# Kernel optimization log

Measured on AMD Instinct MI355X. Metric: run time of the kernel, lower is better.

The kernel has to match this reference:

```python
import jax, jax.numpy as jnp
import numpy as np

# Module hyperparameters (from __init__ defaults / init_kwargs)
A_PLUS = 0.005
A_MINUS = 0.00525
TAU_PLUS = 20.0
TAU_MINUS = 20.0
DT = 1.0

B, T, N_PRE, N_POST = 512, 100, 256, 256
SPIKE_RATE = 0.1


def setup_inputs() -> dict:
    key = jax.random.key(0)
    k1, k2, k3 = jax.random.split(key, 3)
    pre_spikes = (jax.random.uniform(k1, (B, T, N_PRE)) < SPIKE_RATE).astype(jnp.float32)
    post_spikes = (jax.random.uniform(k2, (B, T, N_POST)) < SPIKE_RATE).astype(jnp.float32)
    weights = jax.random.uniform(k3, (N_PRE, N_POST), dtype=jnp.float32)
    return {"pre_spikes": pre_spikes, "post_spikes": post_spikes, "weights": weights}


def _pre_trace(pre_tbn, decay):
    """trace[t] = sum_{tau=1..t} decay^tau * pre[t-tau]  (exact recurrence).

    pre_tbn: [T, B, N]. Returns [T, B, N] with trace[0] = 0.
    """
    def step(carry, x_t):
        # emit trace[t] = carry, then carry' = decay * (carry + pre[t])
        return decay * (carry + x_t), carry
    _, trace = jax.lax.scan(step, jnp.zeros_like(pre_tbn[0]), pre_tbn)
    return trace


def reference(pre_spikes, post_spikes, weights):
    """Classical STDP weight update.

    With T <= int(tau_plus*5) the original nested t/tau loops equal:
      dW[p,q] = (1/(B*T)) * sum_{t,b} (A+ * trace+[t,b,p] - A- * trace-[t,b,p]) * post[b,t,q]
    where trace+/- are exponential pre-synaptic eligibility traces.
    """
    batch, time_steps, _ = pre_spikes.shape
    pre_t = jnp.transpose(pre_spikes, (1, 0, 2))    # [T, B, n_pre]
    post_t = jnp.transpose(post_spikes, (1, 0, 2))  # [T, B, n_post]

    decay_plus = jnp.exp(jnp.float32(-DT / TAU_PLUS))
    decay_minus = jnp.exp(jnp.float32(-DT / TAU_MINUS))

    trace_plus = _pre_trace(pre_t, decay_plus)    # LTP: pre fires before post
    trace_minus = _pre_trace(pre_t, decay_minus)  # LTD: pre fires before post (depression of reversed pairing)

    eff = A_PLUS * trace_plus - A_MINUS * trace_minus  # [T, B, n_pre]
    weight_update = jnp.einsum('tbp,tbq->pq', eff, post_t) / (batch * time_steps)
    # original initializes update as zeros_like(weights); output shape matches weights
    return weight_update + jnp.zeros_like(weights)
```

## Files before the change

kernel.cpp:

```cpp
#include <hip/hip_runtime.h>
#include <stdint.h>

#define B_SZ   512
#define T_SZ   100
#define NPRE   256
#define NPOST  256
#define KTOT   (B_SZ * T_SZ)

typedef __bf16 bf16x8 __attribute__((ext_vector_type(8)));
typedef float  floatx4 __attribute__((ext_vector_type(4)));

__device__ __forceinline__ uint32_t bf16_rne(float v) {
    uint32_t bits = __float_as_uint(v);
    return (bits + 0x7FFFu + ((bits >> 16) & 1u)) >> 16;
}
__device__ __forceinline__ uint32_t pack_trunc2(float a, float b) {
    return (__float_as_uint(a) >> 16) | (__float_as_uint(b) & 0xFFFF0000u);
}

__global__ __launch_bounds__(512) void stdp_fused_gemm(
    const float* __restrict__ pre, const float* __restrict__ post,
    float* __restrict__ partial)
{
    __shared__ __align__(16) unsigned short A_lds[32][512];
    __shared__ __align__(16) unsigned short B_lds[64][512];

    const int bx = blockIdx.x;
    const int s  = bx & 127;
    const int pt = bx >> 7;
    const int tid = threadIdx.x;
    const int lane = tid & 63, wave = tid >> 6;
    const int wp = wave & 3, wq = wave >> 2;
    const int l15 = lane & 15, l4 = lane >> 4;

    const int p_loc = tid & 127, lbo = tid >> 7;
    uint32_t pk[50];
    {
        const int b = s * 4 + lbo;
        const float decay = 0.95122942450071400910f;
        const float* src = pre + (size_t)b * (T_SZ * NPRE) + pt * 128 + p_loc;
        float carry = 0.0f;
#pragma unroll
        for (int kc = 0; kc < 3; ++kc) {
            float x[32];
#pragma unroll
            for (int j = 0; j < 32; ++j)
                x[j] = src[(size_t)(kc * 32 + j) * NPRE];
#pragma unroll
            for (int j = 0; j < 16; ++j) {
                uint32_t lo = bf16_rne(carry);
                carry = decay * (carry + x[2 * j]);
                uint32_t hi = bf16_rne(carry);
                carry = decay * (carry + x[2 * j + 1]);
                pk[kc * 16 + j] = lo | (hi << 16);
            }
        }
        float x[4];
#pragma unroll
        for (int j = 0; j < 4; ++j)
            x[j] = src[(size_t)(96 + j) * NPRE];
#pragma unroll
        for (int j = 0; j < 2; ++j) {
            uint32_t lo = bf16_rne(carry);
            carry = decay * (carry + x[2 * j]);
            uint32_t hi = bf16_rne(carry);
            carry = decay * (carry + x[2 * j + 1]);
            pk[48 + j] = lo | (hi << 16);
        }
    }

    const int q = tid & 255, hh = tid >> 8;
    const int qg = q >> 4, q15 = q & 15;

    floatx4 acc[2][8] = {};

    for (int lb = 0; lb < 4; ++lb) {
        const int b = s * 4 + lb;

        if (lbo == lb) {
            const int pg = p_loc >> 4, lp = p_loc & 15;
#pragma unroll
            for (int kc = 0; kc < 3; ++kc)
#pragma unroll
                for (int l4w = 0; l4w < 4; ++l4w)
                    *(uint4*)&A_lds[kc * 8 + pg][(l4w * 16 + lp) * 8] =
                        make_uint4(pk[kc * 16 + l4w * 4], pk[kc * 16 + l4w * 4 + 1],
                                   pk[kc * 16 + l4w * 4 + 2], pk[kc * 16 + l4w * 4 + 3]);
            *(uint4*)&A_lds[24 + pg][lp * 8] = make_uint4(pk[48], pk[49], 0u, 0u);
#pragma unroll
            for (int l4w = 1; l4w < 4; ++l4w)
                *(uint4*)&A_lds[24 + pg][(l4w * 16 + lp) * 8] =
                    make_uint4(0u, 0u, 0u, 0u);
        }

        const float* pb = post + (size_t)b * (T_SZ * NPOST) + q;
        if (hh == 0) {
#pragma unroll
            for (int half = 0; half < 2; ++half) {
                float x[32];
#pragma unroll
                for (int j = 0; j < 32; ++j)
                    x[j] = pb[(size_t)(half * 32 + j) * NPOST];
#pragma unroll
                for (int o = 0; o < 4; ++o) {
                    int oct = half * 4 + o;
                    uint4 v = make_uint4(pack_trunc2(x[o * 8 + 0], x[o * 8 + 1]),
                                         pack_trunc2(x[o * 8 + 2], x[o * 8 + 3]),
                                         pack_trunc2(x[o * 8 + 4], x[o * 8 + 5]),
                                         pack_trunc2(x[o * 8 + 6], x[o * 8 + 7]));
                    *(uint4*)&B_lds[(oct >> 2) * 16 + qg][(((oct & 3) * 16 + q15)) * 8] = v;
                }
            }
        } else {
            float x[32];
#pragma unroll
            for (int j = 0; j < 32; ++j)
                x[j] = pb[(size_t)(64 + j) * NPOST];
            float y[4];
#pragma unroll
            for (int j = 0; j < 4; ++j)
                y[j] = pb[(size_t)(96 + j) * NPOST];
#pragma unroll
            for (int o = 0; o < 4; ++o) {
                int oct = 8 + o;
                uint4 v = make_uint4(pack_trunc2(x[o * 8 + 0], x[o * 8 + 1]),
                                     pack_trunc2(x[o * 8 + 2], x[o * 8 + 3]),
                                     pack_trunc2(x[o * 8 + 4], x[o * 8 + 5]),
                                     pack_trunc2(x[o * 8 + 6], x[o * 8 + 7]));
                *(uint4*)&B_lds[(oct >> 2) * 16 + qg][(((oct & 3) * 16 + q15)) * 8] = v;
            }
            *(uint4*)&B_lds[3 * 16 + qg][(q15) * 8] =
                make_uint4(pack_trunc2(y[0], y[1]), pack_trunc2(y[2], y[3]), 0u, 0u);
#pragma unroll
            for (int o = 13; o < 16; ++o)
                *(uint4*)&B_lds[3 * 16 + qg][(((o & 3) * 16 + q15)) * 8] =
                    make_uint4(0u, 0u, 0u, 0u);
        }
        __syncthreads();

#pragma unroll
        for (int kc = 0; kc < 4; ++kc) {
            bf16x8 a[2], bb[8];
#pragma unroll
            for (int f = 0; f < 2; ++f)
                a[f] = *(const bf16x8*)&A_lds[kc * 8 + wp * 2 + f][lane * 8];
#pragma unroll
            for (int g = 0; g < 8; ++g)
                bb[g] = *(const bf16x8*)&B_lds[kc * 16 + wq * 8 + g][lane * 8];
#pragma unroll
            for (int f = 0; f < 2; ++f)
#pragma unroll
                for (int g = 0; g < 8; ++g)
                    acc[f][g] = __builtin_amdgcn_mfma_f32_16x16x32_bf16(
                        a[f], bb[g], acc[f][g], 0, 0, 0);
        }
        __syncthreads();
    }

    float* pout = partial + (size_t)bx * (128 * 256);
#pragma unroll
    for (int f = 0; f < 2; ++f) {
        int r0 = wp * 32 + f * 16 + l4 * 4;
#pragma unroll
        for (int g = 0; g < 8; ++g) {
            int c = wq * 128 + g * 16 + l15;
#pragma unroll
            for (int v = 0; v < 4; ++v)
                pout[(size_t)(r0 + v) * 256 + c] = acc[f][g][v];
        }
    }
}

__global__ __launch_bounds__(256) void stdp_reduce1(
    const float* __restrict__ partial, float* __restrict__ tmp)
{
    const int t = blockIdx.x * 256 + threadIdx.x;
    const int g = t >> 16;
    const int e = t & 65535;
    const int pt = e >> 15;
    const float* src = partial + ((size_t)(pt * 128 + g * 16)) * 32768 + (e & 32767);
    float a4[4] = {};
#pragma unroll
    for (int i = 0; i < 4; ++i)
#pragma unroll
        for (int u = 0; u < 4; ++u)
            a4[u] += src[(size_t)(u * 4 + i) * 32768];
    tmp[t] = (a4[0] + a4[1]) + (a4[2] + a4[3]);
}

__global__ __launch_bounds__(256) void stdp_reduce2(
    const float* __restrict__ tmp, float* __restrict__ out)
{
    const int idx = blockIdx.x * 256 + threadIdx.x;
    float a[4];
#pragma unroll
    for (int u = 0; u < 4; ++u)
        a[u] = tmp[(size_t)(2 * u) * 65536 + idx] +
               tmp[(size_t)(2 * u + 1) * 65536 + idx];
    const float scale = (0.005f - 0.00525f) * (1.0f / (float)KTOT);
    out[idx] = ((a[0] + a[1]) + (a[2] + a[3])) * scale;
}

extern "C" void kernel_launch(void* const* d_in, const int* in_sizes, int n_in,
                              void* d_out, int out_size, void* d_ws, size_t ws_size,
                              hipStream_t stream)
{
    const float* pre  = (const float*)d_in[0];
    const float* post = (const float*)d_in[1];
    float* out = (float*)d_out;

    float* partial = (float*)d_ws;
    float* tmp     = (float*)((char*)d_ws + (size_t)33554432);

    stdp_fused_gemm<<<256, 512, 0, stream>>>(pre, post, partial);
    stdp_reduce1<<<2048, 256, 0, stream>>>(partial, tmp);
    stdp_reduce2<<<256, 256, 0, stream>>>(tmp, out);
}
```

Before: 144.6 us.

## Halve B LDS tile and split K loop into two phases for occupancy

The post-spike B tile in LDS is halved by loading and consuming time steps in two phases of 64 and 36 per batch, each followed by two MFMA k-chunks. A launch bound of 4 blocks per CU is added to push register use down. The goal is lower LDS and register footprint per block so more blocks fit per CU, and shorter register live ranges for the loaded post values. In exchange each batch iteration now needs two extra barriers, and the register cap may cause spills given the 50-entry packed trace array.

```diff
diff --git a/kernel.cpp b/kernel.cpp
--- a/kernel.cpp
+++ b/kernel.cpp
@@ -18,12 +18,12 @@
     return (__float_as_uint(a) >> 16) | (__float_as_uint(b) & 0xFFFF0000u);
 }
 
-__global__ __launch_bounds__(512) void stdp_fused_gemm(
+__global__ __launch_bounds__(512, 4) void stdp_fused_gemm(
     const float* __restrict__ pre, const float* __restrict__ post,
     float* __restrict__ partial)
 {
     __shared__ __align__(16) unsigned short A_lds[32][512];
-    __shared__ __align__(16) unsigned short B_lds[64][512];
+    __shared__ __align__(16) unsigned short B_lds[32][512];
 
     const int bx = blockIdx.x;
     const int s  = bx & 127;
@@ -76,6 +76,7 @@
 
     for (int lb = 0; lb < 4; ++lb) {
         const int b = s * 4 + lb;
+        const float* pb = post + (size_t)b * (T_SZ * NPOST) + q;
 
         if (lbo == lb) {
             const int pg = p_loc >> 4, lp = p_loc & 15;
@@ -92,58 +93,69 @@
                 *(uint4*)&A_lds[24 + pg][(l4w * 16 + lp) * 8] =
                     make_uint4(0u, 0u, 0u, 0u);
         }
-
-        const float* pb = post + (size_t)b * (T_SZ * NPOST) + q;
+        {
+            float x[32];
+#pragma unroll
+            for (int j = 0; j < 32; ++j)
+                x[j] = pb[(size_t)(hh * 32 + j) * NPOST];
+#pragma unroll
+            for (int o = 0; o < 4; ++o)
+                *(uint4*)&B_lds[hh * 16 + qg][(o * 16 + q15) * 8] =
+                    make_uint4(pack_trunc2(x[o * 8 + 0], x[o * 8 + 1]),
+                               pack_trunc2(x[o * 8 + 2], x[o * 8 + 3]),
+                               pack_trunc2(x[o * 8 + 4], x[o * 8 + 5]),
+                               pack_trunc2(x[o * 8 + 6], x[o * 8 + 7]));
+        }
+        __syncthreads();
+#pragma unroll
+        for (int kc = 0; kc < 2; ++kc) {
+            bf16x8 a[2], bb[8];
+#pragma unroll
+            for (int f = 0; f < 2; ++f)
+                a[f] = *(const bf16x8*)&A_lds[kc * 8 + wp * 2 + f][lane * 8];
+#pragma unroll
+            for (int g = 0; g < 8; ++g)
+                bb[g] = *(const bf16x8*)&B_lds[kc * 16 + wq * 8 + g][lane * 8];
+#pragma unroll
+            for (int f = 0; f < 2; ++f)
+#pragma unroll
+                for (int g = 0; g < 8; ++g)
+                    acc[f][g] = __builtin_amdgcn_mfma_f32_16x16x32_bf16(
+                        a[f], bb[g], acc[f][g], 0, 0, 0);
+        }
+        __syncthreads();
+
         if (hh == 0) {
-#pragma unroll
-            for (int half = 0; half < 2; ++half) {
-                float x[32];
-#pragma unroll
-                for (int j = 0; j < 32; ++j)
-                    x[j] = pb[(size_t)(half * 32 + j) * NPOST];
-#pragma unroll
-                for (int o = 0; o < 4; ++o) {
-                    int oct = half * 4 + o;
-                    uint4 v = make_uint4(pack_trunc2(x[o * 8 + 0], x[o * 8 + 1]),
-                                         pack_trunc2(x[o * 8 + 2], x[o * 8 + 3]),
-                                         pack_trunc2(x[o * 8 + 4], x[o * 8 + 5]),
-                                         pack_trunc2(x[o * 8 + 6], x[o * 8 + 7]));
-                    *(uint4*)&B_lds[(oct >> 2) * 16 + qg][(((oct & 3) * 16 + q15)) * 8] = v;
-                }
-            }
-        } else {
             float x[32];
 #pragma unroll
             for (int j = 0; j < 32; ++j)
                 x[j] = pb[(size_t)(64 + j) * NPOST];
+#pragma unroll
+            for (int o = 0; o < 4; ++o)
+                *(uint4*)&B_lds[qg][(o * 16 + q15) * 8] =
+                    make_uint4(pack_trunc2(x[o * 8 + 0], x[o * 8 + 1]),
+                               pack_trunc2(x[o * 8 + 2], x[o * 8 + 3]),
+                               pack_trunc2(x[o * 8 + 4], x[o * 8 + 5]),
+                               pack_trunc2(x[o * 8 + 6], x[o * 8 + 7]));
+        } else {
             float y[4];
 #pragma unroll
             for (int j = 0; j < 4; ++j)
                 y[j] = pb[(size_t)(96 + j) * NPOST];
-#pragma unroll
-            for (int o = 0; o < 4; ++o) {
-                int oct = 8 + o;
-                uint4 v = make_uint4(pack_trunc2(x[o * 8 + 0], x[o * 8 + 1]),
-                                     pack_trunc2(x[o * 8 + 2], x[o * 8 + 3]),
-                                     pack_trunc2(x[o * 8 + 4], x[o * 8 + 5]),
-                                     pack_trunc2(x[o * 8 + 6], x[o * 8 + 7]));
-                *(uint4*)&B_lds[(oct >> 2) * 16 + qg][(((oct & 3) * 16 + q15)) * 8] = v;
-            }
-            *(uint4*)&B_lds[3 * 16 + qg][(q15) * 8] =
+            *(uint4*)&B_lds[16 + qg][(q15) * 8] =
                 make_uint4(pack_trunc2(y[0], y[1]), pack_trunc2(y[2], y[3]), 0u, 0u);
 #pragma unroll
-            for (int o = 13; o < 16; ++o)
-                *(uint4*)&B_lds[3 * 16 + qg][(((o & 3) * 16 + q15)) * 8] =
+            for (int o = 1; o < 4; ++o)
+                *(uint4*)&B_lds[16 + qg][(o * 16 + q15) * 8] =
                     make_uint4(0u, 0u, 0u, 0u);
         }
         __syncthreads();
-
-#pragma unroll
-        for (int kc = 0; kc < 4; ++kc) {
+#pragma unroll
+        for (int kc = 0; kc < 2; ++kc) {
             bf16x8 a[2], bb[8];
 #pragma unroll
             for (int f = 0; f < 2; ++f)
-                a[f] = *(const bf16x8*)&A_lds[kc * 8 + wp * 2 + f][lane * 8];
+                a[f] = *(const bf16x8*)&A_lds[(kc + 2) * 8 + wp * 2 + f][lane * 8];
 #pragma unroll
             for (int g = 0; g < 8; ++g)
                 bb[g] = *(const bf16x8*)&B_lds[kc * 16 + wq * 8 + g][lane * 8];
```

Measured after the change: 177.8 us. 22.9% more time.

## Split GEMM into 128x128 output tiles with 256-thread blocks and 2-block occupancy

Applied to the files above, without the earlier changes.

The fused trace+GEMM kernel now uses 512 blocks of 256 threads. Each block computes a 128x128 output tile, with P and Q tiles indexed from the block id, instead of a 128x256 tile. LDS per block is halved and launch bounds request two blocks per CU. The goal is more parallelism and better latency hiding. The cost is that the pre-trace recurrence is recomputed for both Q tiles and threads do two rounds of trace work, with the reduce kernels remapped to the new partial layout.

```diff
diff --git a/kernel.cpp b/kernel.cpp
--- a/kernel.cpp
+++ b/kernel.cpp
@@ -18,155 +18,151 @@
     return (__float_as_uint(a) >> 16) | (__float_as_uint(b) & 0xFFFF0000u);
 }
 
-__global__ __launch_bounds__(512) void stdp_fused_gemm(
+__global__ __launch_bounds__(256, 2) void stdp_fused_gemm(
     const float* __restrict__ pre, const float* __restrict__ post,
     float* __restrict__ partial)
 {
     __shared__ __align__(16) unsigned short A_lds[32][512];
-    __shared__ __align__(16) unsigned short B_lds[64][512];
-
-    const int bx = blockIdx.x;
-    const int s  = bx & 127;
-    const int pt = bx >> 7;
-    const int tid = threadIdx.x;
+    __shared__ __align__(16) unsigned short B_lds[32][512];
+
+    const int bx   = blockIdx.x;
+    const int s    = bx & 127;
+    const int tile = bx >> 7;
+    const int pt   = tile & 1;
+    const int qt   = tile >> 1;
+    const int tid  = threadIdx.x;
     const int lane = tid & 63, wave = tid >> 6;
-    const int wp = wave & 3, wq = wave >> 2;
     const int l15 = lane & 15, l4 = lane >> 4;
 
-    const int p_loc = tid & 127, lbo = tid >> 7;
-    uint32_t pk[50];
-    {
-        const int b = s * 4 + lbo;
-        const float decay = 0.95122942450071400910f;
-        const float* src = pre + (size_t)b * (T_SZ * NPRE) + pt * 128 + p_loc;
-        float carry = 0.0f;
-#pragma unroll
-        for (int kc = 0; kc < 3; ++kc) {
-            float x[32];
-#pragma unroll
-            for (int j = 0; j < 32; ++j)
-                x[j] = src[(size_t)(kc * 32 + j) * NPRE];
-#pragma unroll
-            for (int j = 0; j < 16; ++j) {
+    const int half  = tid >> 7;
+    const int p_loc = tid & 127;
+    const int qloc  = tid & 127;
+    const int qg = qloc >> 4, q15 = qloc & 15;
+
+    const float decay = 0.95122942450071400910f;
+
+    floatx4 acc[2][8] = {};
+
+    for (int r = 0; r < 2; ++r) {
+        uint32_t pk[50];
+        {
+            const int b = s * 4 + 2 * r + half;
+            const float* src = pre + (size_t)b * (T_SZ * NPRE) + pt * 128 + p_loc;
+            float carry = 0.0f;
+#pragma unroll
+            for (int kc = 0; kc < 3; ++kc) {
+                float x[32];
+#pragma unroll
+                for (int j = 0; j < 32; ++j)
+                    x[j] = src[(size_t)(kc * 32 + j) * NPRE];
+#pragma unroll
+                for (int j = 0; j < 16; ++j) {
+                    uint32_t lo = bf16_rne(carry);
+                    carry = decay * (carry + x[2 * j]);
+                    uint32_t hi = bf16_rne(carry);
+                    carry = decay * (carry + x[2 * j + 1]);
+                    pk[kc * 16 + j] = lo | (hi << 16);
+                }
+            }
+            float x[4];
+#pragma unroll
+            for (int j = 0; j < 4; ++j)
+                x[j] = src[(size_t)(96 + j) * NPRE];
+#pragma unroll
+            for (int j = 0; j < 2; ++j) {
                 uint32_t lo = bf16_rne(carry);
                 carry = decay * (carry + x[2 * j]);
                 uint32_t hi = bf16_rne(carry);
                 carry = decay * (carry + x[2 * j + 1]);
-                pk[kc * 16 + j] = lo | (hi << 16);
+                pk[48 + j] = lo | (hi << 16);
             }
         }
-        float x[4];
-#pragma unroll
-        for (int j = 0; j < 4; ++j)
-            x[j] = src[(size_t)(96 + j) * NPRE];
-#pragma unroll
-        for (int j = 0; j < 2; ++j) {
-            uint32_t lo = bf16_rne(carry);
-            carry = decay * (carry + x[2 * j]);
-            uint32_t hi = bf16_rne(carry);
-            carry = decay * (carry + x[2 * j + 1]);
-            pk[48 + j] = lo | (hi << 16);
+
+        for (int lh = 0; lh < 2; ++lh) {
+            const int b = s * 4 + 2 * r + lh;
+
+            if (half == lh) {
+                const int pg = p_loc >> 4, lp = p_loc & 15;
+#pragma unroll
+                for (int kc = 0; kc < 3; ++kc)
+#pragma unroll
+                    for (int w = 0; w < 4; ++w)
+                        *(uint4*)&A_lds[kc * 8 + pg][(w * 16 + lp) * 8] =
+                            make_uint4(pk[kc * 16 + w * 4],     pk[kc * 16 + w * 4 + 1],
+                                       pk[kc * 16 + w * 4 + 2], pk[kc * 16 + w * 4 + 3]);
+                *(uint4*)&A_lds[24 + pg][lp * 8] = make_uint4(pk[48], pk[49], 0u, 0u);
+#pragma unroll
+                for (int w = 1; w < 4; ++w)
+                    *(uint4*)&A_lds[24 + pg][(w * 16 + lp) * 8] =
+                        make_uint4(0u, 0u, 0u, 0u);
+            }
+
+            const float* pb = post + (size_t)b * (T_SZ * NPOST) + qt * 128 + qloc;
+            if (half == 0) {
+                float x[48];
+#pragma unroll
+                for (int j = 0; j < 48; ++j)
+                    x[j] = pb[(size_t)j * NPOST];
+#pragma unroll
+                for (int o = 0; o < 6; ++o)
+                    *(uint4*)&B_lds[(o >> 2) * 8 + qg][((o & 3) * 16 + q15) * 8] =
+                        make_uint4(pack_trunc2(x[o * 8 + 0], x[o * 8 + 1]),
+                                   pack_trunc2(x[o * 8 + 2], x[o * 8 + 3]),
+                                   pack_trunc2(x[o * 8 + 4], x[o * 8 + 5]),
+                                   pack_trunc2(x[o * 8 + 6], x[o * 8 + 7]));
+            } else {
+                float x[52];
+#pragma unroll
+                for (int j = 0; j < 52; ++j)
+                    x[j] = pb[(size_t)(48 + j) * NPOST];
+#pragma unroll
+                for (int o = 6; o < 12; ++o) {
+                    int u = o * 8 - 48;
+                    *(uint4*)&B_lds[(o >> 2) * 8 + qg][((o & 3) * 16 + q15) * 8] =
+                        make_uint4(pack_trunc2(x[u + 0], x[u + 1]),
+                                   pack_trunc2(x[u + 2], x[u + 3]),
+                                   pack_trunc2(x[u + 4], x[u + 5]),
+                                   pack_trunc2(x[u + 6], x[u + 7]));
+                }
+                *(uint4*)&B_lds[24 + qg][q15 * 8] =
+                    make_uint4(pack_trunc2(x[48], x[49]), pack_trunc2(x[50], x[51]), 0u, 0u);
+#pragma unroll
+                for (int o = 13; o < 16; ++o)
+                    *(uint4*)&B_lds[24 + qg][((o & 3) * 16 + q15) * 8] =
+                        make_uint4(0u, 0u, 0u, 0u);
+            }
+            __syncthreads();
+
+#pragma unroll
+            for (int kc = 0; kc < 4; ++kc) {
+                bf16x8 a[2], bb[8];
+#pragma unroll
+                for (int f = 0; f < 2; ++f)
+                    a[f] = *(const bf16x8*)&A_lds[kc * 8 + wave * 2 + f][lane * 8];
+#pragma unroll
+                for (int g = 0; g < 8; ++g)
+                    bb[g] = *(const bf16x8*)&B_lds[kc * 8 + g][lane * 8];
+#pragma unroll
+                for (int f = 0; f < 2; ++f)
+#pragma unroll
+                    for (int g = 0; g < 8; ++g)
+                        acc[f][g] = __builtin_amdgcn_mfma_f32_16x16x32_bf16(
+                            a[f], bb[g], acc[f][g], 0, 0, 0);
+            }
+            __syncthreads();
         }
     }
 
-    const int q = tid & 255, hh = tid >> 8;
-    const int qg = q >> 4, q15 = q & 15;
-
-    floatx4 acc[2][8] = {};
-
-    for (int lb = 0; lb < 4; ++lb) {
-        const int b = s * 4 + lb;
-
-        if (lbo == lb) {
-            const int pg = p_loc >> 4, lp = p_loc & 15;
-#pragma unroll
-            for (int kc = 0; kc < 3; ++kc)
-#pragma unroll
-                for (int l4w = 0; l4w < 4; ++l4w)
-                    *(uint4*)&A_lds[kc * 8 + pg][(l4w * 16 + lp) * 8] =
-                        make_uint4(pk[kc * 16 + l4w * 4], pk[kc * 16 + l4w * 4 + 1],
-                                   pk[kc * 16 + l4w * 4 + 2], pk[kc * 16 + l4w * 4 + 3]);
-            *(uint4*)&A_lds[24 + pg][lp * 8] = make_uint4(pk[48], pk[49], 0u, 0u);
-#pragma unroll
-            for (int l4w = 1; l4w < 4; ++l4w)
-                *(uint4*)&A_lds[24 + pg][(l4w * 16 + lp) * 8] =
-                    make_uint4(0u, 0u, 0u, 0u);
-        }
-
-        const float* pb = post + (size_t)b * (T_SZ * NPOST) + q;
-        if (hh == 0) {
-#pragma unroll
-            for (int half = 0; half < 2; ++half) {
-                float x[32];
-#pragma unroll
-                for (int j = 0; j < 32; ++j)
-                    x[j] = pb[(size_t)(half * 32 + j) * NPOST];
-#pragma unroll
-                for (int o = 0; o < 4; ++o) {
-                    int oct = half * 4 + o;
-                    uint4 v = make_uint4(pack_trunc2(x[o * 8 + 0], x[o * 8 + 1]),
-                                         pack_trunc2(x[o * 8 + 2], x[o * 8 + 3]),
-                                         pack_trunc2(x[o * 8 + 4], x[o * 8 + 5]),
-                                         pack_trunc2(x[o * 8 + 6], x[o * 8 + 7]));
-                    *(uint4*)&B_lds[(oct >> 2) * 16 + qg][(((oct & 3) * 16 + q15)) * 8] = v;
-                }
-            }
-        } else {
-            float x[32];
-#pragma unroll
-            for (int j = 0; j < 32; ++j)
-                x[j] = pb[(size_t)(64 + j) * NPOST];
-            float y[4];
-#pragma unroll
-            for (int j = 0; j < 4; ++j)
-                y[j] = pb[(size_t)(96 + j) * NPOST];
-#pragma unroll
-            for (int o = 0; o < 4; ++o) {
-                int oct = 8 + o;
-                uint4 v = make_uint4(pack_trunc2(x[o * 8 + 0], x[o * 8 + 1]),
-                                     pack_trunc2(x[o * 8 + 2], x[o * 8 + 3]),
-                                     pack_trunc2(x[o * 8 + 4], x[o * 8 + 5]),
-                                     pack_trunc2(x[o * 8 + 6], x[o * 8 + 7]));
-                *(uint4*)&B_lds[(oct >> 2) * 16 + qg][(((oct & 3) * 16 + q15)) * 8] = v;
-            }
-            *(uint4*)&B_lds[3 * 16 + qg][(q15) * 8] =
-                make_uint4(pack_trunc2(y[0], y[1]), pack_trunc2(y[2], y[3]), 0u, 0u);
-#pragma unroll
-            for (int o = 13; o < 16; ++o)
-                *(uint4*)&B_lds[3 * 16 + qg][(((o & 3) * 16 + q15)) * 8] =
-                    make_uint4(0u, 0u, 0u, 0u);
-        }
-        __syncthreads();
-
-#pragma unroll
-        for (int kc = 0; kc < 4; ++kc) {
-            bf16x8 a[2], bb[8];
-#pragma unroll
-            for (int f = 0; f < 2; ++f)
-                a[f] = *(const bf16x8*)&A_lds[kc * 8 + wp * 2 + f][lane * 8];
-#pragma unroll
-            for (int g = 0; g < 8; ++g)
-                bb[g] = *(const bf16x8*)&B_lds[kc * 16 + wq * 8 + g][lane * 8];
-#pragma unroll
-            for (int f = 0; f < 2; ++f)
-#pragma unroll
-                for (int g = 0; g < 8; ++g)
-                    acc[f][g] = __builtin_amdgcn_mfma_f32_16x16x32_bf16(
-                        a[f], bb[g], acc[f][g], 0, 0, 0);
-        }
-        __syncthreads();
-    }
-
-    float* pout = partial + (size_t)bx * (128 * 256);
+    float* pout = partial + (size_t)bx * (128 * 128);
 #pragma unroll
     for (int f = 0; f < 2; ++f) {
-        int r0 = wp * 32 + f * 16 + l4 * 4;
+        int r0 = wave * 32 + f * 16 + l4 * 4;
 #pragma unroll
         for (int g = 0; g < 8; ++g) {
-            int c = wq * 128 + g * 16 + l15;
+            int c = g * 16 + l15;
 #pragma unroll
             for (int v = 0; v < 4; ++v)
-                pout[(size_t)(r0 + v) * 256 + c] = acc[f][g][v];
+                pout[(size_t)(r0 + v) * 128 + c] = acc[f][g][v];
         }
     }
 }
@@ -177,14 +173,14 @@
     const int t = blockIdx.x * 256 + threadIdx.x;
     const int g = t >> 16;
     const int e = t & 65535;
-    const int pt = e >> 15;
-    const float* src = partial + ((size_t)(pt * 128 + g * 16)) * 32768 + (e & 32767);
+    const int tile = e >> 14;
+    const float* src = partial + ((size_t)(tile * 128 + g * 16) << 14) + (e & 16383);
     float a4[4] = {};
 #pragma unroll
     for (int i = 0; i < 4; ++i)
 #pragma unroll
         for (int u = 0; u < 4; ++u)
-            a4[u] += src[(size_t)(u * 4 + i) * 32768];
+            a4[u] += src[(size_t)(u * 4 + i) << 14];
     tmp[t] = (a4[0] + a4[1]) + (a4[2] + a4[3]);
 }
 
@@ -192,11 +188,14 @@
     const float* __restrict__ tmp, float* __restrict__ out)
 {
     const int idx = blockIdx.x * 256 + threadIdx.x;
+    const int P = idx >> 8, Q = idx & 255;
+    const int tile = (Q >> 7) * 2 + (P >> 7);
+    const int e = (tile << 14) | ((P & 127) << 7) | (Q & 127);
     float a[4];
 #pragma unroll
     for (int u = 0; u < 4; ++u)
-        a[u] = tmp[(size_t)(2 * u) * 65536 + idx] +
-               tmp[(size_t)(2 * u + 1) * 65536 + idx];
+        a[u] = tmp[(size_t)(2 * u) * 65536 + e] +
+               tmp[(size_t)(2 * u + 1) * 65536 + e];
     const float scale = (0.005f - 0.00525f) * (1.0f / (float)KTOT);
     out[idx] = ((a[0] + a[1]) + (a[2] + a[3])) * scale;
 }
@@ -212,7 +211,7 @@
     float* partial = (float*)d_ws;
     float* tmp     = (float*)((char*)d_ws + (size_t)33554432);
 
-    stdp_fused_gemm<<<256, 512, 0, stream>>>(pre, post, partial);
+    stdp_fused_gemm<<<512, 256, 0, stream>>>(pre, post, partial);
     stdp_reduce1<<<2048, 256, 0, stream>>>(partial, tmp);
     stdp_reduce2<<<256, 256, 0, stream>>>(tmp, out);
 }
```

Measured after the change: 142.2 us. About the same (-1.7%).
